# Optimization experiments

Measured on AMD Instinct MI355X. Metric: run time of the kernel, lower is better.

Reference implementation:

```python
import jax, jax.numpy as jnp
import numpy as np
import math

NEG = -1e9


def maximum_path(neg_cent, text_len, spec_len):
    # neg_cent: [B, Ts, Tt]; monotonic alignment (Viterbi) DP as in VITS.
    B, Ts, Tt = neg_cent.shape
    jj = jnp.arange(Tt)
    tt = jnp.arange(Ts)
    node_mask = (jj[None, None, :] < text_len[:, None, None]) & (tt[None, :, None] < spec_len[:, None, None])
    nc = jnp.where(node_mask, neg_cent, NEG)

    def fstep(q, nc_t):
        # q: [B, Tt] best score ending at text index j at previous frame
        q_shift = jnp.concatenate([jnp.full((B, 1), NEG, q.dtype), q[:, :-1]], axis=1)
        d = q_shift >= q  # True -> came from j-1 (diagonal move)
        q_new = nc_t + jnp.maximum(q, q_shift)
        return q_new, d

    q0 = jnp.broadcast_to(jnp.where(jj == 0, 0.0, NEG), (B, Tt)).astype(neg_cent.dtype)
    _, dirs = jax.lax.scan(fstep, q0, jnp.swapaxes(nc, 0, 1))  # dirs: [Ts, B, Tt]

    def bstep(j, inp):
        t, d_t = inp
        start = (t == spec_len - 1)
        j_eff = jnp.where(start, text_len - 1, j)
        valid = t < spec_len
        emit = ((jj[None, :] == j_eff[:, None]) & valid[:, None]).astype(neg_cent.dtype)
        came_diag = jnp.take_along_axis(d_t, j_eff[:, None], axis=1)[:, 0]
        j_next = jnp.where(valid, jnp.maximum(j_eff - came_diag.astype(j_eff.dtype), 0), j_eff)
        return j_next, emit

    j_init = jnp.zeros((B,), text_len.dtype)
    _, path = jax.lax.scan(bstep, j_init, (jnp.arange(Ts), dirs), reverse=True)
    return jnp.swapaxes(path, 0, 1)  # [B, Ts, Tt]


def setup_inputs() -> dict:
    B, C, Ts, Tt = 16, 192, 2048, 512
    key = jax.random.key(0)
    k1, k2, k3, k4, k5 = jax.random.split(key, 5)
    z_p = jax.random.normal(k1, (B, C, Ts), dtype=jnp.float32)
    m_p = jax.random.normal(k2, (B, C, Tt), dtype=jnp.float32)
    logs_p = 0.1 * jax.random.normal(k3, (B, C, Tt), dtype=jnp.float32)
    text_len = jax.random.randint(k4, (B,), Tt // 2, Tt + 1, dtype=jnp.int32)
    extra = jax.random.randint(k5, (B,), 0, Ts - Tt + 1, dtype=jnp.int32)
    spec_len = jnp.minimum(text_len + extra, Ts)
    return {"z_p": z_p, "m_p": m_p, "logs_p": logs_p, "spec_len": spec_len, "text_len": text_len}


def reference(z_p, m_p, logs_p, spec_len, text_len):
    B, C, Ts = z_p.shape
    Tt = m_p.shape[2]
    text_mask = (jnp.arange(Tt)[None, :] < text_len[:, None]).astype(z_p.dtype)[:, None, :]  # [B,1,Tt]
    spec_mask = (jnp.arange(Ts)[None, :] < spec_len[:, None]).astype(z_p.dtype)[:, None, :]  # [B,1,Ts]

    # --- neg_cent (torch.no_grad block) ---
    s_p_sq_r = jnp.exp(-2.0 * logs_p)  # [B,C,Tt]
    neg_cent1 = jnp.sum(-0.5 * math.log(2.0 * math.pi) - logs_p, axis=1, keepdims=True)  # [B,1,Tt]
    neg_cent2 = jnp.einsum('bct,bcu->btu', -0.5 * z_p ** 2, s_p_sq_r)  # [B,Ts,Tt]
    neg_cent3 = jnp.einsum('bct,bcu->btu', z_p, m_p * s_p_sq_r)  # [B,Ts,Tt]
    neg_cent4 = jnp.sum(-0.5 * m_p ** 2 * s_p_sq_r, axis=1, keepdims=True)  # [B,1,Tt]
    neg_cent = neg_cent1 + neg_cent2 + neg_cent3 + neg_cent4

    path = jax.lax.stop_gradient(maximum_path(neg_cent, text_len, spec_len))  # [B,Ts,Tt]

    duration = jnp.sum(path, axis=1)[:, None, :]  # [B,1,Tt]
    logw_ = jnp.log(duration + 1e-6) * text_mask  # [B,1,Tt]

    # expand prior stats along the alignment path: [B,C,Ts]
    m_p_exp = jnp.einsum('btu,bcu->bct', path, m_p)
    logs_p_exp = jnp.einsum('btu,bcu->bct', path, logs_p)

    return (path, duration, logw_, m_p_exp, logs_p_exp, text_mask, spec_mask)
```

## Files before the change

### kernel.cpp

```cpp
#include <hip/hip_runtime.h>
#include <hip/hip_bf16.h>
#include <math.h>

#define BB 16
#define CC 192
#define TS 2048
#define TT 512
#define KK 384

#define OFF_PATH 0
#define OFF_DUR  (16777216)
#define OFF_LOGW (OFF_DUR + 8192)
#define OFF_MEXP (OFF_LOGW + 8192)
#define OFF_LEXP (OFF_MEXP + 6291456)
#define OFF_TMASK (OFF_LEXP + 6291456)
#define OFF_SMASK (OFF_TMASK + 8192)

#define NEGCF (-1e9f)

__global__ __launch_bounds__(512) void vits_prep(
    const float* __restrict__ m_p, const float* __restrict__ logs_p,
    const int* __restrict__ spec_len, const int* __restrict__ text_len,
    float* __restrict__ Bmat, float* __restrict__ avec,
    float* __restrict__ tmask, float* __restrict__ smask)
{
    const int uc = blockIdx.x;
    const int b  = blockIdx.y;
    const int tid = threadIdx.x;
    const int ul = tid & 31;
    const int cg = tid >> 5;
    const int u = uc*32 + ul;
    const float C0 = -0.91893853320467274178f;
    float a_acc = 0.f;
    for (int c = cg; c < CC; c += 16) {
        float lg = logs_p[((size_t)b*CC + c)*TT + u];
        float mm = m_p[((size_t)b*CC + c)*TT + u];
        float s  = expf(-2.f*lg);
        float ms = mm * s;
        Bmat[((size_t)b*KK + 2*c    )*TT + u] = ms;
        Bmat[((size_t)b*KK + 2*c + 1)*TT + u] = s;
        a_acc += C0 - lg - 0.5f*mm*ms;
    }
    __shared__ float red[16][33];
    red[cg][ul] = a_acc;
    __syncthreads();
    #pragma unroll
    for (int s = 8; s > 0; s >>= 1) {
        if (cg < s) red[cg][ul] += red[cg + s][ul];
        __syncthreads();
    }
    if (cg == 0) {
        avec[b*TT + u] = red[0][ul];
        tmask[b*TT + u] = (u < text_len[b]) ? 1.f : 0.f;
    }
    if (tid < 128) {
        int t = uc*128 + tid;
        smask[b*TS + t] = (t < spec_len[b]) ? 1.f : 0.f;
    }
}

__global__ __launch_bounds__(256) void vits_gemm(
    const float* __restrict__ z, const float* __restrict__ Bmat,
    const float* __restrict__ avec, float* __restrict__ out)
{
    const int b  = blockIdx.z;
    const int t0 = blockIdx.y * 128;
    const int u0 = blockIdx.x * 128;
    __shared__ float As[8][128];
    __shared__ float Bs[8][128];
    const int tid = threadIdx.x;
    const int tx = tid & 15, ty = tid >> 4;
    float acc[8][8] = {};
    const float* zb = z    + (size_t)b * CC * TS;
    const float* Bb = Bmat + (size_t)b * KK * TT;

    const int c_l = tid >> 6;
    const int t_l = (tid & 63) * 2;
    const int k_b = tid >> 5;
    const int u_l = (tid & 31) * 4;

    float2 zr = *(const float2*)(zb + (size_t)c_l*TS + t0 + t_l);
    float4 br = *(const float4*)(Bb + (size_t)k_b*TT + u0 + u_l);

    for (int kc = 0; kc < KK/8; ++kc) {
        *(float2*)&As[2*c_l  ][t_l] = make_float2(zr.x, zr.y);
        *(float2*)&As[2*c_l+1][t_l] = make_float2(-0.5f*zr.x*zr.x, -0.5f*zr.y*zr.y);
        *(float4*)&Bs[k_b][u_l] = br;
        __syncthreads();
        if (kc + 1 < KK/8) {
            zr = *(const float2*)(zb + (size_t)((kc+1)*4 + c_l)*TS + t0 + t_l);
            br = *(const float4*)(Bb + (size_t)((kc+1)*8 + k_b)*TT + u0 + u_l);
        }
        #pragma unroll
        for (int k = 0; k < 8; ++k) {
            float4 a0 = *(const float4*)&As[k][ty*4];
            float4 a1 = *(const float4*)&As[k][ty*4 + 64];
            float4 b0 = *(const float4*)&Bs[k][tx*4];
            float4 b1 = *(const float4*)&Bs[k][tx*4 + 64];
            float aa[8] = {a0.x,a0.y,a0.z,a0.w,a1.x,a1.y,a1.z,a1.w};
            float bb[8] = {b0.x,b0.y,b0.z,b0.w,b1.x,b1.y,b1.z,b1.w};
            #pragma unroll
            for (int i = 0; i < 8; ++i)
                #pragma unroll
                for (int j = 0; j < 8; ++j)
                    acc[i][j] += aa[i]*bb[j];
        }
        __syncthreads();
    }

    float4 ab0 = *(const float4*)(avec + b*TT + u0 + tx*4);
    float4 ab1 = *(const float4*)(avec + b*TT + u0 + tx*4 + 64);
    float ab[8] = {ab0.x,ab0.y,ab0.z,ab0.w,ab1.x,ab1.y,ab1.z,ab1.w};
    #pragma unroll
    for (int i = 0; i < 8; ++i) {
        int tt = t0 + ((i < 4) ? (ty*4 + i) : (64 + ty*4 + (i-4)));
        float* orow = out + (size_t)((size_t)b*TS + tt)*TT + u0;
        float4 o0, o1;
        o0.x = acc[i][0] + ab[0]; o0.y = acc[i][1] + ab[1];
        o0.z = acc[i][2] + ab[2]; o0.w = acc[i][3] + ab[3];
        o1.x = acc[i][4] + ab[4]; o1.y = acc[i][5] + ab[5];
        o1.z = acc[i][6] + ab[6]; o1.w = acc[i][7] + ab[7];
        *(float4*)(orow + tx*4)      = o0;
        *(float4*)(orow + tx*4 + 64) = o1;
    }
}

__device__ __forceinline__ float dpp_ror1_f32(float v) {
    union { float f; int i; } u, r;
    u.f = v;
    r.i = __builtin_amdgcn_update_dpp(0, u.i, 0x13C, 0xF, 0xF, false);
    return r.f;
}

#define DIRS(j,w) dirs[((j)<<6) | ((w) ^ ((j) & 31))]

__global__ __launch_bounds__(512, 1) void vits_dp(
    const float* __restrict__ nc,
    const int* __restrict__ spec_len, const int* __restrict__ text_len,
    float* __restrict__ dur, float* __restrict__ logw, int* __restrict__ jt)
{
    __shared__ unsigned int dirs[TT*(TS/32)];
    __shared__ float bq[8][256];
    __shared__ int prog[8];
    __shared__ int Tr[TT + 1];

    const int tid  = threadIdx.x;
    const int lane = tid & 63;
    const int wid  = tid >> 6;
    const int b = blockIdx.x;
    const int SL = spec_len[b], TL = text_len[b];
    const int col = (wid << 6) + lane;
    const bool l0  = (lane == 0);
    const bool l63 = (lane == 63);

    float q = (col == 0) ? 0.0f : NEGCF;
    unsigned int bits = 0;

    const float* ncb = nc + (size_t)b*TS*TT + col;
    float pf[16];
    #pragma unroll
    for (int i = 0; i < 16; ++i) pf[i] = ncb[(size_t)i*TT];
    const float* pcur = ncb + (size_t)16*TT;

    for (int i = tid; i < 8*256; i += 512) ((float*)bq)[i] = NEGCF;
    if (tid < 8) prog[tid] = 0;
    __syncthreads();

    volatile int* vprog = (volatile int*)prog;
    const int nch = SL >> 5;

    for (int c = 0; c < nch; ++c) {
        if (wid > 0) { while (vprog[wid-1] < c+1) __builtin_amdgcn_s_sleep(1); }
        if (wid < 7 && c > 6) { while (vprog[wid+1] < c-6) __builtin_amdgcn_s_sleep(1); }
        asm volatile("" ::: "memory");

        float4 R[9];
        R[0] = *(const float4*)&bq[wid][(c*32 + 252) & 255];
        #pragma unroll
        for (int g = 1; g < 9; ++g)
            R[g] = *(const float4*)&bq[wid][(c*32 + (g-1)*4) & 255];

        float4 wbuf;
        #pragma unroll
        for (int s = 0; s < 32; ++s) {
            float f = pf[s & 15];
            pf[s & 15] = *pcur;
            pcur += TT;
            float B = ((const float*)&R[(s+3) >> 2])[(s+3) & 3];
            float qr = dpp_ror1_f32(q);
            float qprev = l0 ? B : qr;
            bool d = (qprev >= q);
            bits = (bits << 1) | (unsigned)d;
            q = f + fmaxf(qprev, q);
            ((float*)&wbuf)[s & 3] = q;
            if ((s & 3) == 3) {
                if (l63 && wid < 7)
                    *(float4*)&bq[wid+1][(c*32 + s - 3) & 255] = wbuf;
            }
        }
        DIRS(col, c) = bits;
        bits = 0;
        asm volatile("s_waitcnt lgkmcnt(0)" ::: "memory");
        if (l0) vprog[wid] = c + 1;
    }

    const int rem = SL & 31;
    if (rem) {
        if (wid > 0) { while (vprog[wid-1] < nch+1) __builtin_amdgcn_s_sleep(1); }
        asm volatile("" ::: "memory");
        for (int t = nch*32; t < SL; ++t) {
            float f = ncb[(size_t)t*TT];
            float B = *(volatile float*)&bq[wid][(t-1) & 255];
            float qr = dpp_ror1_f32(q);
            float qprev = l0 ? B : qr;
            bool d = (qprev >= q);
            bits = (bits << 1) | (unsigned)d;
            q = f + fmaxf(qprev, q);
            if (l63 && wid < 7) *(volatile float*)&bq[wid+1][t & 255] = q;
            asm volatile("s_waitcnt lgkmcnt(0)" ::: "memory");
        }
        DIRS(col, SL >> 5) = bits << (32 - rem);
        asm volatile("s_waitcnt lgkmcnt(0)" ::: "memory");
        if (l0) vprog[wid] = nch + 1;
    }
    __syncthreads();

    for (int i = tid; i <= TT; i += 512) Tr[i] = 0;
    __syncthreads();

    if (tid == 0) {
        Tr[TL] = SL;
        int j = TL - 1, tc = SL - 1;
        while (j > 0 && tc >= 0) {
            int w = tc >> 5;
            int bcur = 31 - (tc & 31);
            unsigned int W = DIRS(j, w) & (0xFFFFFFFFu << bcur);
            if (W) {
                int bp = __ffs(W) - 1;
                int tp = (w << 5) + 31 - bp;
                Tr[j] = tp;
                --j;
                tc = tp - 1;
            } else {
                if (w == 0) break;
                tc = (w << 5) - 1;
            }
        }
    }
    __syncthreads();

    for (int u = tid; u < TT; u += 512) {
        float dv = (u < TL) ? (float)(Tr[u+1] - Tr[u]) : 0.0f;
        dur[b*TT + u] = dv;
        logw[b*TT + u] = (u < TL) ? logf(dv + 1e-6f) : 0.0f;
    }
    for (int u = 0; u < TL; ++u) {
        int t1 = Tr[u+1];
        for (int t = Tr[u] + tid; t < t1; t += 512) jt[b*TS + t] = u;
    }
    for (int t = SL + tid; t < TS; t += 512) jt[b*TS + t] = -1;
}

__global__ void vits_path(const int* __restrict__ jt, float4* __restrict__ path)
{
    int idx = blockIdx.x*blockDim.x + threadIdx.x;
    const int total = BB*TS*(TT/4);
    for (; idx < total; idx += gridDim.x*blockDim.x) {
        int u4 = idx & (TT/4 - 1);
        int bt = idx >> 7;
        int j = jt[bt];
        float4 v = make_float4(0.f,0.f,0.f,0.f);
        int r = j - (u4 << 2);
        if (r >= 0 && r < 4) ((float*)&v)[r] = 1.f;
        path[idx] = v;
    }
}

__global__ void vits_mlexp(const int* __restrict__ jt,
    const float* __restrict__ m_p, const float* __restrict__ logs_p,
    float4* __restrict__ mexp, float4* __restrict__ lexp)
{
    int idx = blockIdx.x*blockDim.x + threadIdx.x;
    const int total = BB*CC*(TS/4);
    for (; idx < total; idx += gridDim.x*blockDim.x) {
        int t4 = idx & (TS/4 - 1);
        int bc = idx >> 9;
        int b = bc / CC;
        int4 jv = *(const int4*)(jt + b*TS + (t4 << 2));
        const float* mrow = m_p    + (size_t)bc*TT;
        const float* lrow = logs_p + (size_t)bc*TT;
        float4 mv, lv;
        mv.x = (jv.x >= 0) ? mrow[jv.x] : 0.f;  lv.x = (jv.x >= 0) ? lrow[jv.x] : 0.f;
        mv.y = (jv.y >= 0) ? mrow[jv.y] : 0.f;  lv.y = (jv.y >= 0) ? lrow[jv.y] : 0.f;
        mv.z = (jv.z >= 0) ? mrow[jv.z] : 0.f;  lv.z = (jv.z >= 0) ? lrow[jv.z] : 0.f;
        mv.w = (jv.w >= 0) ? mrow[jv.w] : 0.f;  lv.w = (jv.w >= 0) ? lrow[jv.w] : 0.f;
        mexp[idx] = mv;
        lexp[idx] = lv;
    }
}

extern "C" void kernel_launch(void* const* d_in, const int* in_sizes, int n_in,
                              void* d_out, int out_size, void* d_ws, size_t ws_size,
                              hipStream_t stream) {
    const float* z_p      = (const float*)d_in[0];
    const float* m_p      = (const float*)d_in[1];
    const float* logs_p   = (const float*)d_in[2];
    const int*   spec_len = (const int*)d_in[3];
    const int*   text_len = (const int*)d_in[4];
    float* out = (float*)d_out;

    float* Bmat = (float*)d_ws;
    float* avec = Bmat + (size_t)BB*KK*TT;
    int*   jt   = (int*)(avec + BB*TT);

    float* path  = out + OFF_PATH;
    float* dur   = out + OFF_DUR;
    float* logw  = out + OFF_LOGW;
    float* mexp  = out + OFF_MEXP;
    float* lexp  = out + OFF_LEXP;
    float* tmask = out + OFF_TMASK;
    float* smask = out + OFF_SMASK;

    vits_prep<<<dim3(16, BB), 512, 0, stream>>>(m_p, logs_p, spec_len, text_len,
                                                Bmat, avec, tmask, smask);
    vits_gemm<<<dim3(TT/128, TS/128, BB), 256, 0, stream>>>(z_p, Bmat, avec, path);
    vits_dp<<<BB, 512, 0, stream>>>(path, spec_len, text_len, dur, logw, jt);
    vits_path<<<2048, 256, 0, stream>>>(jt, (float4*)path);
    vits_mlexp<<<2048, 256, 0, stream>>>(jt, m_p, logs_p, (float4*)mexp, (float4*)lexp);
}
```

Baseline: 426.4 us.

## Split Viterbi DP into per-wave blocks with global-memory flag handoff

```diff
diff --git a/kernel.cpp b/kernel.cpp
--- a/kernel.cpp
+++ b/kernel.cpp
@@ -132,59 +132,66 @@
     return r.f;
 }
 
-#define DIRS(j,w) dirs[((j)<<6) | ((w) ^ ((j) & 31))]
-
-__global__ __launch_bounds__(512, 1) void vits_dp(
-    const float* __restrict__ nc,
-    const int* __restrict__ spec_len, const int* __restrict__ text_len,
-    float* __restrict__ dur, float* __restrict__ logw, int* __restrict__ jt)
-{
-    __shared__ unsigned int dirs[TT*(TS/32)];
-    __shared__ float bq[8][256];
-    __shared__ int prog[8];
-    __shared__ int Tr[TT + 1];
-
-    const int tid  = threadIdx.x;
-    const int lane = tid & 63;
-    const int wid  = tid >> 6;
-    const int b = blockIdx.x;
-    const int SL = spec_len[b], TL = text_len[b];
-    const int col = (wid << 6) + lane;
-    const bool l0  = (lane == 0);
-    const bool l63 = (lane == 63);
+__global__ void vits_zero(int* __restrict__ flags)
+{
+    if (threadIdx.x < 128) flags[threadIdx.x] = 0;
+}
+
+#define RINGF 32
+
+__global__ __launch_bounds__(64, 1) void vits_dpfwd(
+    const float* __restrict__ nc, const int* __restrict__ spec_len,
+    float* __restrict__ bbuf, int* __restrict__ flags,
+    unsigned int* __restrict__ dirs_g)
+{
+    const int w = blockIdx.x;
+    const int b = blockIdx.y;
+    const int lane = threadIdx.x;
+    const int SL = spec_len[b];
+    const int col = (w << 6) + lane;
+    const bool l0 = (lane == 0), l63 = (lane == 63);
 
     float q = (col == 0) ? 0.0f : NEGCF;
     unsigned int bits = 0;
 
     const float* ncb = nc + (size_t)b*TS*TT + col;
-    float pf[16];
+    float pf[RINGF];
     #pragma unroll
-    for (int i = 0; i < 16; ++i) pf[i] = ncb[(size_t)i*TT];
-    const float* pcur = ncb + (size_t)16*TT;
-
-    for (int i = tid; i < 8*256; i += 512) ((float*)bq)[i] = NEGCF;
-    if (tid < 8) prog[tid] = 0;
-    __syncthreads();
-
-    volatile int* vprog = (volatile int*)prog;
+    for (int i = 0; i < RINGF; ++i) pf[i] = ncb[(size_t)i*TT];
+    const float* pcur = ncb + (size_t)RINGF*TT;
+
+    float* bb_out       = bbuf + ((b<<3) + w    )*2052 + 4;
+    const float* bb_in  = bbuf + ((b<<3) + w - 1)*2052 + 4;
+    int* myflag   = flags + (b<<3) + w;
+    int* leftflag = flags + (b<<3) + w - 1;
+
     const int nch = SL >> 5;
 
     for (int c = 0; c < nch; ++c) {
-        if (wid > 0) { while (vprog[wid-1] < c+1) __builtin_amdgcn_s_sleep(1); }
-        if (wid < 7 && c > 6) { while (vprog[wid+1] < c-6) __builtin_amdgcn_s_sleep(1); }
-        asm volatile("" ::: "memory");
-
+        if (w > 0) {
+            while (__hip_atomic_load(leftflag, __ATOMIC_ACQUIRE, __HIP_MEMORY_SCOPE_AGENT) < c + 1)
+                __builtin_amdgcn_s_sleep(1);
+        }
         float4 R[9];
-        R[0] = *(const float4*)&bq[wid][(c*32 + 252) & 255];
-        #pragma unroll
-        for (int g = 1; g < 9; ++g)
-            R[g] = *(const float4*)&bq[wid][(c*32 + (g-1)*4) & 255];
-
-        float4 wbuf;
+        if (w > 0 && c > 0) {
+            const float* bi = bb_in + (c << 5);
+            R[0] = *(const float4*)(bi - 4);
+            #pragma unroll
+            for (int g = 1; g < 9; ++g) R[g] = *(const float4*)(bi + (g-1)*4);
+        } else if (w > 0) {
+            R[0] = make_float4(NEGCF,NEGCF,NEGCF,NEGCF);
+            const float* bi = bb_in;
+            #pragma unroll
+            for (int g = 1; g < 9; ++g) R[g] = *(const float4*)(bi + (g-1)*4);
+        } else {
+            #pragma unroll
+            for (int g = 0; g < 9; ++g) R[g] = make_float4(NEGCF,NEGCF,NEGCF,NEGCF);
+        }
+        float4 wb;
         #pragma unroll
         for (int s = 0; s < 32; ++s) {
-            float f = pf[s & 15];
-            pf[s & 15] = *pcur;
+            float f = pf[s & (RINGF-1)];
+            pf[s & (RINGF-1)] = *pcur;
             pcur += TT;
             float B = ((const float*)&R[(s+3) >> 2])[(s+3) & 3];
             float qr = dpp_ror1_f32(q);
@@ -192,36 +199,59 @@
             bool d = (qprev >= q);
             bits = (bits << 1) | (unsigned)d;
             q = f + fmaxf(qprev, q);
-            ((float*)&wbuf)[s & 3] = q;
-            if ((s & 3) == 3) {
-                if (l63 && wid < 7)
-                    *(float4*)&bq[wid+1][(c*32 + s - 3) & 255] = wbuf;
-            }
-        }
-        DIRS(col, c) = bits;
+            ((float*)&wb)[s & 3] = q;
+            if ((s & 3) == 3 && l63 && w < 7)
+                *(float4*)(bb_out + (c << 5) + s - 3) = wb;
+        }
+        dirs_g[((size_t)b << 15) + (c << 9) + col] = bits;
         bits = 0;
-        asm volatile("s_waitcnt lgkmcnt(0)" ::: "memory");
-        if (l0) vprog[wid] = c + 1;
-    }
-
+        if (w < 7) {
+            asm volatile("s_waitcnt vmcnt(0)" ::: "memory");
+            if (l63) __hip_atomic_store(myflag, c + 1, __ATOMIC_RELEASE, __HIP_MEMORY_SCOPE_AGENT);
+        }
+    }
     const int rem = SL & 31;
     if (rem) {
-        if (wid > 0) { while (vprog[wid-1] < nch+1) __builtin_amdgcn_s_sleep(1); }
-        asm volatile("" ::: "memory");
+        if (w > 0) {
+            while (__hip_atomic_load(leftflag, __ATOMIC_ACQUIRE, __HIP_MEMORY_SCOPE_AGENT) < nch + 1)
+                __builtin_amdgcn_s_sleep(1);
+        }
         for (int t = nch*32; t < SL; ++t) {
             float f = ncb[(size_t)t*TT];
-            float B = *(volatile float*)&bq[wid][(t-1) & 255];
+            float B = (w > 0) ? bb_in[t-1] : NEGCF;
             float qr = dpp_ror1_f32(q);
             float qprev = l0 ? B : qr;
             bool d = (qprev >= q);
             bits = (bits << 1) | (unsigned)d;
             q = f + fmaxf(qprev, q);
-            if (l63 && wid < 7) *(volatile float*)&bq[wid+1][t & 255] = q;
-            asm volatile("s_waitcnt lgkmcnt(0)" ::: "memory");
-        }
-        DIRS(col, SL >> 5) = bits << (32 - rem);
-        asm volatile("s_waitcnt lgkmcnt(0)" ::: "memory");
-        if (l0) vprog[wid] = nch + 1;
+            if (l63 && w < 7) bb_out[t] = q;
+        }
+        dirs_g[((size_t)b << 15) + (nch << 9) + col] = bits << (32 - rem);
+    }
+    if (w < 7) {
+        asm volatile("s_waitcnt vmcnt(0)" ::: "memory");
+        if (l63) __hip_atomic_store(myflag, nch + 2, __ATOMIC_RELEASE, __HIP_MEMORY_SCOPE_AGENT);
+    }
+}
+
+#define DIRS(j,w) dirs[((j)<<6) | ((w) ^ ((j) & 31))]
+
+__global__ __launch_bounds__(512) void vits_dpbt(
+    const unsigned int* __restrict__ dirs_g,
+    const int* __restrict__ spec_len, const int* __restrict__ text_len,
+    float* __restrict__ dur, float* __restrict__ logw, int* __restrict__ jt)
+{
+    __shared__ unsigned int dirs[TT*(TS/32)];
+    __shared__ int Tr[TT + 1];
+    const int b = blockIdx.x;
+    const int tid = threadIdx.x;
+    const int SL = spec_len[b], TL = text_len[b];
+    const unsigned int* dg = dirs_g + ((size_t)b << 15);
+
+    const int nwin = (SL + 31) >> 5;
+    for (int i = tid; i < (nwin << 9); i += 512) {
+        int c = i >> 9, col = i & 511;
+        DIRS(col, c) = dg[i];
     }
     __syncthreads();
 
@@ -321,10 +351,16 @@
     float* tmask = out + OFF_TMASK;
     float* smask = out + OFF_SMASK;
 
+    unsigned int* dirs_g = (unsigned int*)mexp;
+    float* bbuf  = lexp;
+    int*   flags = (int*)(lexp + 300000);
+
+    vits_zero<<<1, 128, 0, stream>>>(flags);
     vits_prep<<<dim3(16, BB), 512, 0, stream>>>(m_p, logs_p, spec_len, text_len,
                                                 Bmat, avec, tmask, smask);
     vits_gemm<<<dim3(TT/128, TS/128, BB), 256, 0, stream>>>(z_p, Bmat, avec, path);
-    vits_dp<<<BB, 512, 0, stream>>>(path, spec_len, text_len, dur, logw, jt);
+    vits_dpfwd<<<dim3(8, BB), 64, 0, stream>>>(path, spec_len, bbuf, flags, dirs_g);
+    vits_dpbt<<<BB, 512, 0, stream>>>(dirs_g, spec_len, text_len, dur, logw, jt);
     vits_path<<<2048, 256, 0, stream>>>(jt, (float4*)path);
     vits_mlexp<<<2048, 256, 0, stream>>>(jt, m_p, logs_p, (float4*)mexp, (float4*)lexp);
 }
```

New measurement: 546.5 us. +28.2%, slower.
